# Performance work log

Hardware: AMD Instinct MI355X
Metric: run time of the kernel (lower is better)

Reference implementation:

```python
import jax, jax.numpy as jnp
import numpy as np
import math

L = 6; D = 768; NH = 12; DH = D // NH; V = 2048; CTX = 512; B = 16; T = 512
PAD_ID = 0; PAD_X = 18; PAD_Y = 32; N_ACTIONS = 9


def _layernorm(x, s, b, eps=1e-5):
    m = jnp.mean(x, axis=-1, keepdims=True)
    v = jnp.mean((x - m) ** 2, axis=-1, keepdims=True)
    return (x - m) * jax.lax.rsqrt(v + eps) * s + b


def setup_inputs() -> dict:
    key = jax.random.key(0)
    ks = jax.random.split(key, 16)
    s = 0.02
    x_emb = jax.random.normal(ks[4], (19, D), jnp.float32) * s
    x_emb = x_emb.at[PAD_X].set(0.0)  # padding_idx row is zero in torch
    y_emb = jax.random.normal(ks[5], (33, D), jnp.float32) * s
    y_emb = y_emb.at[PAD_Y].set(0.0)
    return {
        "history_cards": jax.random.randint(ks[0], (B, T), 0, V),
        "history_players": jax.random.randint(ks[1], (B, T), 0, 2),
        "deck": jax.random.randint(ks[2], (B, 8), 0, V),
        "opp_deck": jax.random.randint(ks[3], (B, 8), 0, V),
        "tok_emb": jax.random.normal(ks[6], (V, D), jnp.float32) * s,
        "player_emb": jax.random.normal(ks[7], (2, D), jnp.float32) * s,
        "pos_emb": jax.random.normal(ks[8], (CTX, D), jnp.float32) * s,
        "x_emb": x_emb,
        "y_emb": y_emb,
        "ln1_s": jnp.ones((L, D), jnp.float32),
        "ln1_b": jnp.zeros((L, D), jnp.float32),
        "qkv_w": jax.random.normal(ks[9], (L, D, 3 * D), jnp.float32) * s,
        "qkv_b": jnp.zeros((L, 3 * D), jnp.float32),
        "proj_w": jax.random.normal(ks[10], (L, D, D), jnp.float32) * s,
        "proj_b": jnp.zeros((L, D), jnp.float32),
        "ln2_s": jnp.ones((L, D), jnp.float32),
        "ln2_b": jnp.zeros((L, D), jnp.float32),
        "fc1_w": jax.random.normal(ks[11], (L, D, 4 * D), jnp.float32) * s,
        "fc1_b": jnp.zeros((L, 4 * D), jnp.float32),
        "fc2_w": jax.random.normal(ks[12], (L, 4 * D, D), jnp.float32) * s,
        "fc2_b": jnp.zeros((L, D), jnp.float32),
        "lnf_s": jnp.ones((D,), jnp.float32),
        "lnf_b": jnp.zeros((D,), jnp.float32),
        "head_w": jax.random.normal(ks[13], (D, N_ACTIONS), jnp.float32) * s,
        "head_b": jnp.zeros((N_ACTIONS,), jnp.float32),
    }


def reference(history_cards, history_players, deck, opp_deck,
              tok_emb, player_emb, pos_emb, x_emb, y_emb,
              ln1_s, ln1_b, qkv_w, qkv_b, proj_w, proj_b,
              ln2_s, ln2_b, fc1_w, fc1_b, fc2_w, fc2_b,
              lnf_s, lnf_b, head_w, head_b):
    Bc, Tc = history_cards.shape
    attn_mask = history_cards != PAD_ID                      # (B,T) True = valid
    all_pad = ~jnp.any(attn_mask, axis=1)
    attn_mask = attn_mask.at[:, 0].set(attn_mask[:, 0] | all_pad)

    # multi-embedding sum (history_x/history_y are None => padding rows = 0)
    h = (tok_emb[history_cards]
         + player_emb[jnp.clip(history_players, 0, 1)]
         + x_emb[PAD_X] + y_emb[PAD_Y]
         + jnp.mean(tok_emb[deck], axis=1, keepdims=True)
         + jnp.mean(tok_emb[opp_deck], axis=1, keepdims=True))
    x = h + pos_emb[:Tc][None]                               # (B,T,D)

    causal = jnp.tril(jnp.ones((Tc, Tc), bool))
    mask = causal[None, None, :, :] & attn_mask[:, None, None, :]  # (B,1,T,T)
    neg_inf = jnp.float32(-jnp.inf)
    scale = 1.0 / math.sqrt(DH)

    for i in range(L):
        # attention
        xn = _layernorm(x, ln1_s[i], ln1_b[i])
        qkv = xn @ qkv_w[i] + qkv_b[i]
        q, k, v = jnp.split(qkv, 3, axis=-1)
        q = q.reshape(Bc, Tc, NH, DH)
        k = k.reshape(Bc, Tc, NH, DH)
        v = v.reshape(Bc, Tc, NH, DH)
        scores = jnp.einsum('bihd,bjhd->bhij', q, k) * scale
        scores = jnp.where(mask, scores, neg_inf)
        w = jax.nn.softmax(scores, axis=-1)
        w = jnp.nan_to_num(w, nan=0.0, posinf=0.0, neginf=0.0)
        y = jnp.einsum('bhij,bjhd->bihd', w, v).reshape(Bc, Tc, D)
        x = x + (y @ proj_w[i] + proj_b[i])
        # MLP
        xn = _layernorm(x, ln2_s[i], ln2_b[i])
        hmid = jax.nn.gelu(xn @ fc1_w[i] + fc1_b[i], approximate=False)
        x = x + (hmid @ fc2_w[i] + fc2_b[i])

    x = _layernorm(x, lnf_s, lnf_b)
    last_idx = jnp.clip(jnp.sum(attn_mask.astype(jnp.int32), axis=1) - 1, 0, None)
    last_h = x[jnp.arange(Bc), last_idx]                     # (B,D)
    return last_h @ head_w + head_b                          # (B,9)
```

## Files before the change

### kernel.cpp

```cpp
#include <hip/hip_runtime.h>
#include <hip/hip_bf16.h>
#include <math.h>

typedef __hip_bfloat16 bf16;
typedef __bf16 bf16x8 __attribute__((ext_vector_type(8)));
typedef float f32x4 __attribute__((ext_vector_type(4)));

__device__ __forceinline__ float b2f(bf16 v){ return __bfloat162float(v); }
__device__ __forceinline__ bf16  f2b(float v){ return __float2bfloat16(v); }

__device__ __forceinline__ float gelu_f(float v){
    float y = v * (1.f + 0.044715f * v * v);
    return v / (1.f + __expf(-1.5957691216057308f * y));
}

__device__ __forceinline__ void gl_lds16(const bf16* g, bf16* l) {
    __builtin_amdgcn_global_load_lds((const __attribute__((address_space(1))) unsigned int*)g,
                                     (__attribute__((address_space(3))) unsigned int*)l, 16, 0, 0);
}

__device__ __forceinline__ uint2 pack4bf(const float* v){
    union { unsigned short e[4]; uint2 u; } pk;
    #pragma unroll
    for (int r = 0; r < 4; r++) pk.e[r] = __builtin_bit_cast(unsigned short, f2b(v[r]));
    return pk.u;
}

__device__ __forceinline__ void phase_bar() {
    __builtin_amdgcn_sched_barrier(0);
    __builtin_amdgcn_s_barrier();
    __builtin_amdgcn_sched_barrier(0);
}

__global__ __launch_bounds__(256) void deckmean_k(const int* __restrict__ deck, const int* __restrict__ opp,
                                                  const float* __restrict__ tok, float* __restrict__ deckm)
{
    int b = blockIdx.x, w = blockIdx.y;
    const int* dk = (w ? opp : deck) + b * 8;
    int idx[8];
    #pragma unroll
    for (int j = 0; j < 8; j++) idx[j] = dk[j];
    float* out = deckm + (size_t)(w * 16 + b) * 768;
    for (int d = threadIdx.x; d < 768; d += 256) {
        float s = 0.f;
        #pragma unroll
        for (int j = 0; j < 8; j++) s += tok[(size_t)idx[j] * 768 + d];
        out[d] = s * 0.125f;
    }
}

__global__ __launch_bounds__(512) void mask_k(const int* __restrict__ cards, int* __restrict__ maskb,
                                              int* __restrict__ lastidx)
{
    int b = blockIdx.x, t = threadIdx.x;
    int m = (cards[b * 512 + t] != 0) ? 1 : 0;
    maskb[b * 512 + t] = m;
    __shared__ int red[512];
    red[t] = m; __syncthreads();
    for (int st = 256; st > 0; st >>= 1) { if (t < st) red[t] += red[t + st]; __syncthreads(); }
    if (t == 0) {
        int cnt = red[0];
        if (cnt == 0) { maskb[b * 512] = 1; cnt = 1; }
        lastidx[b] = cnt - 1;
    }
}

__global__ __launch_bounds__(256) void embed_k(const int* __restrict__ cards, const int* __restrict__ players,
                                               const float* __restrict__ tok, const float* __restrict__ pemb,
                                               const float* __restrict__ pos, const float* __restrict__ deckm,
                                               float* __restrict__ x)
{
    int t = blockIdx.x;
    int b = t >> 9, ti = t & 511;
    int cd = cards[t];
    int p = players[t]; p = p < 0 ? 0 : (p > 1 ? 1 : p);
    const float* tr  = tok  + (size_t)cd * 768;
    const float* pr  = pemb + (size_t)p  * 768;
    const float* po  = pos  + (size_t)ti * 768;
    const float* dm = deckm + (size_t)b * 768;
    const float* om = deckm + (size_t)(16 + b) * 768;
    float* xr = x + (size_t)t * 768;
    for (int d = threadIdx.x; d < 768; d += 256)
        xr[d] = tr[d] + pr[d] + po[d] + dm[d] + om[d];
}

__global__ __launch_bounds__(192) void ln_k(const float* __restrict__ x, const float* __restrict__ s,
                                            const float* __restrict__ b, bf16* __restrict__ out)
{
    int row = blockIdx.x, tid = threadIdx.x;
    float4 v = ((const float4*)(x + (size_t)row * 768))[tid];
    float sum = v.x + v.y + v.z + v.w;
    float sq  = v.x * v.x + v.y * v.y + v.z * v.z + v.w * v.w;
    #pragma unroll
    for (int off = 32; off > 0; off >>= 1) {
        sum += __shfl_xor(sum, off, 64);
        sq  += __shfl_xor(sq,  off, 64);
    }
    __shared__ float red[6];
    int wv = tid >> 6;
    if ((tid & 63) == 0) { red[wv] = sum; red[3 + wv] = sq; }
    __syncthreads();
    float S = red[0] + red[1] + red[2];
    float Q = red[3] + red[4] + red[5];
    float mean = S * (1.f / 768.f);
    float var  = Q * (1.f / 768.f) - mean * mean;
    float rstd = rsqrtf(var + 1e-5f);
    float4 sv = ((const float4*)s)[tid];
    float4 bv = ((const float4*)b)[tid];
    float o[4] = { (v.x - mean) * rstd * sv.x + bv.x, (v.y - mean) * rstd * sv.y + bv.y,
                   (v.z - mean) * rstd * sv.z + bv.z, (v.w - mean) * rstd * sv.w + bv.w };
    ((uint2*)(out + (size_t)row * 768))[tid] = pack4bf(o);
}

__global__ __launch_bounds__(256) void transpose4_k(const float* __restrict__ qw, const float* __restrict__ pw,
                                                    const float* __restrict__ f1, const float* __restrict__ f2,
                                                    bf16* __restrict__ oq, bf16* __restrict__ op,
                                                    bf16* __restrict__ o1, bf16* __restrict__ o2)
{
    int t = blockIdx.x;
    const float* in; bf16* out; int K, N, nbx;
    if (t < 432)       { in = qw; out = oq; K = 768;  N = 2304; nbx = 36; }
    else if (t < 576)  { in = pw; out = op; K = 768;  N = 768;  t -= 432;  nbx = 12; }
    else if (t < 1152) { in = f1; out = o1; K = 768;  N = 3072; t -= 576;  nbx = 48; }
    else               { in = f2; out = o2; K = 3072; N = 768;  t -= 1152; nbx = 12; }
    int n0 = (t % nbx) * 64, k0 = (t / nbx) * 64;
    int kq = threadIdx.x & 15, nq = threadIdx.x >> 4;
    float4 rr[4];
    #pragma unroll
    for (int r = 0; r < 4; r++)
        rr[r] = *(const float4*)&in[(size_t)(k0 + kq * 4 + r) * N + n0 + nq * 4];
    const float* fp = (const float*)rr;
    #pragma unroll
    for (int c = 0; c < 4; c++) {
        float v[4] = { fp[c], fp[4 + c], fp[8 + c], fp[12 + c] };
        *(uint2*)&out[(size_t)(n0 + nq * 4 + c) * K + k0 + kq * 4] = pack4bf(v);
    }
}

__global__ __launch_bounds__(512, 2) void gemm256_k(const bf16* __restrict__ A, const bf16* __restrict__ BT,
                                                    const float* __restrict__ bias, bf16* __restrict__ out,
                                                    int N, int K, int act, int nbn)
{
    __shared__ __align__(16) bf16 Asb[2][256 * 64];
    __shared__ __align__(16) bf16 Bsb[2][256 * 64];

    const int tid  = threadIdx.x;
    const int lane = tid & 63, wid = tid >> 6;
    const int quad = lane >> 4, l16 = lane & 15;
    const int wr = wid >> 2, wc = wid & 3;
    const int xr  = l16 & 7;
    const int cg0 = quad ^ xr;
    const int cg1 = cg0 ^ 4;

    const int nwg  = gridDim.x;
    const int wgid = ((int)blockIdx.x & 7) * (nwg >> 3) + ((int)blockIdx.x >> 3);
    const int mt = wgid / nbn, nt = wgid - mt * nbn;
    const int m0 = mt * 256, n0 = nt * 256;

    const int srow = wid * 8 + (lane >> 3);
    const int scg  = (lane & 7) ^ (lane >> 3);
    const bf16* sa[4]; const bf16* sb[4];
    #pragma unroll
    for (int s = 0; s < 4; s++) {
        sa[s] = A  + (size_t)(m0 + s * 64 + srow) * K + scg * 8;
        sb[s] = BT + (size_t)(n0 + s * 64 + srow) * K + scg * 8;
    }

#define STG_A(s, b) gl_lds16(sa[s], &Asb[b][((s) * 64 + wid * 8) * 64])
#define STG_B(s, b) gl_lds16(sb[s], &Bsb[b][((s) * 64 + wid * 8) * 64])
#define LD_B(cg) { _Pragma("unroll") for (int ni = 0; ni < 4; ni++) \
    bfv[ni] = __builtin_bit_cast(bf16x8, *(const uint4*)&Bc[(wc * 64 + ni * 16 + l16) * 64 + (cg) * 8]); }
#define LD_A(rb, cg) { _Pragma("unroll") for (int mi = 0; mi < 4; mi++) \
    afv[mi] = __builtin_bit_cast(bf16x8, *(const uint4*)&Ac[(wr * 128 + (rb) + mi * 16 + l16) * 64 + (cg) * 8]); }
#define MFMA16(MB) { _Pragma("unroll") for (int mi = 0; mi < 4; mi++) \
    _Pragma("unroll") for (int ni = 0; ni < 4; ni++) \
        acc[(MB) + mi][ni] = __builtin_amdgcn_mfma_f32_16x16x32_bf16(bfv[ni], afv[mi], acc[(MB) + mi][ni], 0, 0, 0); }

    STG_A(0, 0); STG_A(2, 0);
    STG_B(0, 0); STG_B(1, 0); STG_B(2, 0); STG_B(3, 0);
    STG_A(1, 0); STG_A(3, 0);
    #pragma unroll
    for (int s = 0; s < 4; s++) { sa[s] += 64; sb[s] += 64; }

    f32x4 acc[8][4] = {};

    asm volatile("s_waitcnt vmcnt(2)" ::: "memory");
    phase_bar();

    const int NKT = K >> 6;
    for (int kt = 0; kt < NKT; kt++) {
        const bf16* Ac = Asb[kt & 1];
        const bf16* Bc = Bsb[kt & 1];
        const int nxt = (kt & 1) ^ 1;
        const bool pf = (kt + 1 < NKT);
        bf16x8 bfv[4], afv[4];

        LD_B(cg0); LD_A(0, cg0);
        if (pf) {
            STG_A(0, nxt); STG_A(2, nxt);
            STG_B(0, nxt); STG_B(1, nxt); STG_B(2, nxt); STG_B(3, nxt);
            asm volatile("s_waitcnt vmcnt(6)" ::: "memory");
        } else {
            asm volatile("s_waitcnt vmcnt(0)" ::: "memory");
        }
        phase_bar();
        __builtin_amdgcn_s_setprio(1); MFMA16(0); __builtin_amdgcn_s_setprio(0);
        phase_bar();

        LD_A(64, cg0);
        if (pf) { STG_A(1, nxt); STG_A(3, nxt); }
        phase_bar();
        __builtin_amdgcn_s_setprio(1); MFMA16(4); __builtin_amdgcn_s_setprio(0);
        phase_bar();

        LD_B(cg1); LD_A(0, cg1);
        phase_bar();
        __builtin_amdgcn_s_setprio(1); MFMA16(0); __builtin_amdgcn_s_setprio(0);
        phase_bar();

        LD_A(64, cg1);
        phase_bar();
        __builtin_amdgcn_s_setprio(1); MFMA16(4); __builtin_amdgcn_s_setprio(0);
        asm volatile("s_waitcnt vmcnt(2)" ::: "memory");
        phase_bar();

        #pragma unroll
        for (int s = 0; s < 4; s++) { sa[s] += 64; sb[s] += 64; }
    }

    float4 bv[4];
    #pragma unroll
    for (int ni = 0; ni < 4; ni++)
        bv[ni] = *(const float4*)&bias[n0 + wc * 64 + ni * 16 + quad * 4];

    #pragma unroll
    for (int mi = 0; mi < 8; mi++) {
        const int m = m0 + wr * 128 + mi * 16 + l16;
        #pragma unroll
        for (int ni = 0; ni < 4; ni++) {
            const int nb2 = n0 + wc * 64 + ni * 16 + quad * 4;
            float v[4] = { acc[mi][ni][0] + bv[ni].x, acc[mi][ni][1] + bv[ni].y,
                           acc[mi][ni][2] + bv[ni].z, acc[mi][ni][3] + bv[ni].w };
            if (act) {
                #pragma unroll
                for (int r = 0; r < 4; r++) v[r] = gelu_f(v[r]);
            }
            *(uint2*)&out[(size_t)m * N + nb2] = pack4bf(v);
        }
    }
#undef STG_A
#undef STG_B
#undef LD_B
#undef LD_A
#undef MFMA16
}

__global__ __launch_bounds__(512, 2) void gemmn128_k(const bf16* __restrict__ A, const bf16* __restrict__ BT,
                                                     const float* __restrict__ bias, float* __restrict__ x,
                                                     int N, int K, int nbn)
{
    __shared__ __align__(16) bf16 Asb[3][256 * 64];
    __shared__ __align__(16) bf16 Bsb[3][128 * 64];

    const int tid  = threadIdx.x;
    const int lane = tid & 63, wid = tid >> 6;
    const int quad = lane >> 4, l16 = lane & 15;
    const int wr = wid >> 1, wc = wid & 1;
    const int cg0 = quad ^ (l16 & 7);
    const int cg1 = cg0 ^ 4;

    const int nwg  = gridDim.x;
    const int wgid = ((int)blockIdx.x & 7) * (nwg >> 3) + ((int)blockIdx.x >> 3);
    const int mt = wgid / nbn, nt = wgid - mt * nbn;
    const int m0 = mt * 256, n0 = nt * 128;

    const int srow = wid * 8 + (lane >> 3);
    const int scg  = (lane & 7) ^ (lane >> 3);
    const bf16* sa[4]; const bf16* sb[2];
    #pragma unroll
    for (int s = 0; s < 4; s++) sa[s] = A  + (size_t)(m0 + s * 64 + srow) * K + scg * 8;
    #pragma unroll
    for (int s = 0; s < 2; s++) sb[s] = BT + (size_t)(n0 + s * 64 + srow) * K + scg * 8;

#define NSTG_A(s, b) gl_lds16(sa[s], &Asb[b][((s) * 64 + wid * 8) * 64])
#define NSTG_B(s, b) gl_lds16(sb[s], &Bsb[b][((s) * 64 + wid * 8) * 64])
#define NSTG6(b) { NSTG_A(0, b); NSTG_A(1, b); NSTG_A(2, b); NSTG_A(3, b); NSTG_B(0, b); NSTG_B(1, b); }
#define NADV { _Pragma("unroll") for (int s = 0; s < 4; s++) sa[s] += 64; sb[0] += 64; sb[1] += 64; }
#define NLD(cg, b) { _Pragma("unroll") for (int i = 0; i < 4; i++) { \
    bfv[i] = __builtin_bit_cast(bf16x8, *(const uint4*)&Bsb[b][(wc * 64 + i * 16 + l16) * 64 + (cg) * 8]); \
    afv[i] = __builtin_bit_cast(bf16x8, *(const uint4*)&Asb[b][(wr * 64 + i * 16 + l16) * 64 + (cg) * 8]); } }
#define NMFMA { _Pragma("unroll") for (int mi = 0; mi < 4; mi++) \
    _Pragma("unroll") for (int ni = 0; ni < 4; ni++) \
        acc[mi][ni] = __builtin_amdgcn_mfma_f32_16x16x32_bf16(bfv[ni], afv[mi], acc[mi][ni], 0, 0, 0); }
#define NITER(CUR, ST) { \
    const bool pf = (kt + 2 < NKT); \
    NLD(cg0, CUR); \
    if (pf) { NSTG6(ST); NADV; } \
    phase_bar(); \
    __builtin_amdgcn_s_setprio(1); NMFMA; __builtin_amdgcn_s_setprio(0); \
    phase_bar(); \
    NLD(cg1, CUR); \
    phase_bar(); \
    __builtin_amdgcn_s_setprio(1); NMFMA; __builtin_amdgcn_s_setprio(0); \
    if (pf)               { asm volatile("s_waitcnt vmcnt(6)" ::: "memory"); phase_bar(); } \
    else if (kt + 1 < NKT){ asm volatile("s_waitcnt vmcnt(0)" ::: "memory"); phase_bar(); } \
    kt++; \
}

    f32x4 acc[4][4] = {};
    const int NKT = K >> 6;

    NSTG6(0); NADV;
    NSTG6(1); NADV;
    asm volatile("s_waitcnt vmcnt(6)" ::: "memory");
    phase_bar();

    int kt = 0;
    bf16x8 bfv[4], afv[4];
    #pragma unroll 1
    for (int kt3 = 0; kt3 < NKT; kt3 += 3) {
        NITER(0, 2);
        NITER(1, 0);
        NITER(2, 1);
    }

    float4 bv4[4];
    #pragma unroll
    for (int ni = 0; ni < 4; ni++)
        bv4[ni] = *(const float4*)&bias[n0 + wc * 64 + ni * 16 + quad * 4];

    #pragma unroll
    for (int mi = 0; mi < 4; mi++) {
        const int m = m0 + wr * 64 + mi * 16 + l16;
        #pragma unroll
        for (int ni = 0; ni < 4; ni++) {
            const int nb2 = n0 + wc * 64 + ni * 16 + quad * 4;
            float* xp = &x[(size_t)m * N + nb2];
            float4 xo = *(float4*)xp;
            xo.x += acc[mi][ni][0] + bv4[ni].x;
            xo.y += acc[mi][ni][1] + bv4[ni].y;
            xo.z += acc[mi][ni][2] + bv4[ni].z;
            xo.w += acc[mi][ni][3] + bv4[ni].w;
            *(float4*)xp = xo;
        }
    }
#undef NSTG_A
#undef NSTG_B
#undef NSTG6
#undef NADV
#undef NLD
#undef NMFMA
#undef NITER
}

__global__ __launch_bounds__(256) void attn_k(const bf16* __restrict__ qkv, const int* __restrict__ mask,
                                              bf16* __restrict__ y)
{
    const int qt = blockIdx.x, h = blockIdx.y, b = blockIdx.z;
    const int qbase = qt * 128, tokb = b * 512;
    __shared__ __align__(16) unsigned short Kl[128][72];
    __shared__ __align__(16) unsigned short Vt[64][136];
    __shared__ __align__(16) unsigned short Ptq[4][16][136];
    __shared__ float mkf[128];

    const int tid = threadIdx.x, wave = tid >> 6, lane = tid & 63;
    const int quad = lane >> 4, l16 = lane & 15;

    bf16x8 bq[2][2];
    #pragma unroll
    for (int qc = 0; qc < 2; qc++) {
        const bf16* qp = &qkv[(size_t)(tokb + qbase + wave * 32 + qc * 16 + l16) * 2304 + h * 64];
        bq[qc][0] = __builtin_bit_cast(bf16x8, *(const uint4*)(qp + quad * 8));
        bq[qc][1] = __builtin_bit_cast(bf16x8, *(const uint4*)(qp + 32 + quad * 8));
    }

    float m_i[2] = { -INFINITY, -INFINITY }, l_i[2] = { 0.f, 0.f };
    f32x4 Oacc[2][4] = {};

    const int nst = qt + 1;
    for (int s = 0; s < nst; s++) {
        const int j0 = s * 128;
        __syncthreads();
        {
            int key = tid >> 1, c0 = (tid & 1) * 32;
            const bf16* kg = &qkv[(size_t)(tokb + j0 + key) * 2304 + 768  + h * 64 + c0];
            const bf16* vg = &qkv[(size_t)(tokb + j0 + key) * 2304 + 1536 + h * 64 + c0];
            #pragma unroll
            for (int q = 0; q < 4; q++)
                *(uint4*)&Kl[key][c0 + q * 8] = *(const uint4*)(kg + q * 8);
            union { uint4 u[4]; unsigned short e[32]; } vv;
            #pragma unroll
            for (int q = 0; q < 4; q++) vv.u[q] = *(const uint4*)(vg + q * 8);
            #pragma unroll
            for (int j = 0; j < 32; j++) Vt[c0 + j][key] = vv.e[j];
            if (tid < 128) mkf[tid] = mask[b * 512 + j0 + tid] ? 0.f : -INFINITY;
        }
        __syncthreads();

        #pragma unroll
        for (int qc = 0; qc < 2; qc++) {
            const int qi = qbase + wave * 32 + qc * 16 + l16;

            f32x4 sc[8] = {};
            #pragma unroll
            for (int kcc = 0; kcc < 8; kcc++) {
                bf16x8 af0 = __builtin_bit_cast(bf16x8, *(const uint4*)&Kl[kcc * 16 + l16][quad * 8]);
                bf16x8 af1 = __builtin_bit_cast(bf16x8, *(const uint4*)&Kl[kcc * 16 + l16][32 + quad * 8]);
                sc[kcc] = __builtin_amdgcn_mfma_f32_16x16x32_bf16(af0, bq[qc][0], sc[kcc], 0, 0, 0);
                sc[kcc] = __builtin_amdgcn_mfma_f32_16x16x32_bf16(af1, bq[qc][1], sc[kcc], 0, 0, 0);
            }

            float pv[8][4];
            float mx = -INFINITY;
            #pragma unroll
            for (int kcc = 0; kcc < 8; kcc++) {
                float4 mk4 = *(const float4*)&mkf[kcc * 16 + quad * 4];
                float mkr[4] = { mk4.x, mk4.y, mk4.z, mk4.w };
                #pragma unroll
                for (int r = 0; r < 4; r++) {
                    int krel = kcc * 16 + quad * 4 + r;
                    float sval = (j0 + krel <= qi) ? (sc[kcc][r] * 0.125f + mkr[r]) : -INFINITY;
                    pv[kcc][r] = sval;
                    mx = fmaxf(mx, sval);
                }
            }
            mx = fmaxf(mx, __shfl_xor(mx, 16, 64));
            mx = fmaxf(mx, __shfl_xor(mx, 32, 64));
            float mn = fmaxf(m_i[qc], mx);
            float alpha = (mn == -INFINITY) ? 1.f : __expf(m_i[qc] - mn);
            float lsum = 0.f;
            #pragma unroll
            for (int kcc = 0; kcc < 8; kcc++)
                #pragma unroll
                for (int r = 0; r < 4; r++) {
                    float pp = (pv[kcc][r] == -INFINITY) ? 0.f : __expf(pv[kcc][r] - mn);
                    pv[kcc][r] = pp; lsum += pp;
                }
            lsum += __shfl_xor(lsum, 16, 64);
            lsum += __shfl_xor(lsum, 32, 64);
            m_i[qc] = mn; l_i[qc] = alpha * l_i[qc] + lsum;

            #pragma unroll
            for (int kcc = 0; kcc < 8; kcc++)
                *(uint2*)&Ptq[wave][l16][kcc * 16 + quad * 4] = pack4bf(pv[kcc]);
            #pragma unroll
            for (int mc = 0; mc < 4; mc++)
                #pragma unroll
                for (int r = 0; r < 4; r++) Oacc[qc][mc][r] *= alpha;

            __syncthreads();

            #pragma unroll
            for (int kcc = 0; kcc < 4; kcc++) {
                bf16x8 pb = __builtin_bit_cast(bf16x8, *(const uint4*)&Ptq[wave][l16][kcc * 32 + quad * 8]);
                #pragma unroll
                for (int mc = 0; mc < 4; mc++) {
                    bf16x8 vf = __builtin_bit_cast(bf16x8, *(const uint4*)&Vt[mc * 16 + l16][kcc * 32 + quad * 8]);
                    Oacc[qc][mc] = __builtin_amdgcn_mfma_f32_16x16x32_bf16(vf, pb, Oacc[qc][mc], 0, 0, 0);
                }
            }
        }
    }

    #pragma unroll
    for (int qc = 0; qc < 2; qc++) {
        float inv = (l_i[qc] > 0.f) ? 1.f / l_i[qc] : 0.f;
        const int tok = tokb + qbase + wave * 32 + qc * 16 + l16;
        #pragma unroll
        for (int mc = 0; mc < 4; mc++) {
            float v[4] = { Oacc[qc][mc][0] * inv, Oacc[qc][mc][1] * inv,
                           Oacc[qc][mc][2] * inv, Oacc[qc][mc][3] * inv };
            *(uint2*)&y[(size_t)tok * 768 + h * 64 + mc * 16 + quad * 4] = pack4bf(v);
        }
    }
}

__global__ __launch_bounds__(256) void head_k(const float* __restrict__ x, const int* __restrict__ lastidx,
                                              const float* __restrict__ ls, const float* __restrict__ lb,
                                              const float* __restrict__ hw, const float* __restrict__ hb,
                                              float* __restrict__ out)
{
    int b = blockIdx.x, tid = threadIdx.x;
    const float* xr = x + ((size_t)(b * 512 + lastidx[b])) * 768;
    float v0 = xr[tid], v1 = xr[tid + 256], v2 = xr[tid + 512];
    __shared__ float rs[256], rq[256];
    rs[tid] = v0 + v1 + v2; rq[tid] = v0 * v0 + v1 * v1 + v2 * v2;
    __syncthreads();
    for (int st = 128; st > 0; st >>= 1) {
        if (tid < st) { rs[tid] += rs[tid + st]; rq[tid] += rq[tid + st]; }
        __syncthreads();
    }
    float mean = rs[0] * (1.f / 768.f);
    float var  = rq[0] * (1.f / 768.f) - mean * mean;
    float rstd = rsqrtf(var + 1e-5f);
    float part[9];
    #pragma unroll
    for (int a = 0; a < 9; a++) part[a] = 0.f;
    float vv[3] = { v0, v1, v2 };
    #pragma unroll
    for (int e = 0; e < 3; e++) {
        int d = tid + e * 256;
        float xnv = (vv[e] - mean) * rstd * ls[d] + lb[d];
        #pragma unroll
        for (int a = 0; a < 9; a++) part[a] += xnv * hw[d * 9 + a];
    }
    __shared__ float r9[9][256];
    #pragma unroll
    for (int a = 0; a < 9; a++) r9[a][tid] = part[a];
    __syncthreads();
    for (int st = 128; st > 0; st >>= 1) {
        if (tid < st) {
            for (int a = 0; a < 9; a++) r9[a][tid] += r9[a][tid + st];
        }
        __syncthreads();
    }
    if (tid < 9) out[b * 9 + tid] = r9[tid][0] + hb[tid];
}

extern "C" void kernel_launch(void* const* d_in, const int* in_sizes, int n_in,
                              void* d_out, int out_size, void* d_ws, size_t ws_size,
                              hipStream_t stream) {
    const int*   cards   = (const int*)  d_in[0];
    const int*   players = (const int*)  d_in[1];
    const int*   deck    = (const int*)  d_in[2];
    const int*   oppd    = (const int*)  d_in[3];
    const float* tok     = (const float*)d_in[4];
    const float* pemb    = (const float*)d_in[5];
    const float* pos     = (const float*)d_in[6];
    const float* ln1s  = (const float*)d_in[9];
    const float* ln1b  = (const float*)d_in[10];
    const float* qkvw  = (const float*)d_in[11];
    const float* qkvb  = (const float*)d_in[12];
    const float* projw = (const float*)d_in[13];
    const float* projb = (const float*)d_in[14];
    const float* ln2s  = (const float*)d_in[15];
    const float* ln2b  = (const float*)d_in[16];
    const float* fc1w  = (const float*)d_in[17];
    const float* fc1b  = (const float*)d_in[18];
    const float* fc2w  = (const float*)d_in[19];
    const float* fc2b  = (const float*)d_in[20];
    const float* lnfs  = (const float*)d_in[21];
    const float* lnfb  = (const float*)d_in[22];
    const float* hw    = (const float*)d_in[23];
    const float* hb    = (const float*)d_in[24];
    float* out = (float*)d_out;

    char* p = (char*)d_ws;
    auto alloc = [&](size_t bytes) { char* q = p; p += (bytes + 255) & ~((size_t)255); return q; };
    float* x     = (float*)alloc(8192ull * 768 * 4);
    bf16*  xn    = (bf16*) alloc(8192ull * 768 * 2);
    bf16*  big   = (bf16*) alloc(8192ull * 3072 * 2);
    bf16*  wt    = (bf16*) alloc(7077888ull * 2);
    float* deckm = (float*)alloc(2ull * 16 * 768 * 4);
    int*   maskb = (int*)  alloc(8192ull * 4);
    int*   lasti = (int*)  alloc(64);

    bf16* wq = wt;
    bf16* wp = wq + 2304ull * 768;
    bf16* w1 = wp + 768ull * 768;
    bf16* w2 = w1 + 3072ull * 768;

    deckmean_k<<<dim3(16, 2), 256, 0, stream>>>(deck, oppd, tok, deckm);
    mask_k<<<16, 512, 0, stream>>>(cards, maskb, lasti);
    embed_k<<<8192, 256, 0, stream>>>(cards, players, tok, pemb, pos, deckm, x);

    for (int i = 0; i < 6; i++) {
        transpose4_k<<<1728, 256, 0, stream>>>(
            qkvw + (size_t)i * 768 * 2304, projw + (size_t)i * 768 * 768,
            fc1w + (size_t)i * 768 * 3072, fc2w + (size_t)i * 3072 * 768,
            wq, wp, w1, w2);

        ln_k<<<8192, 192, 0, stream>>>(x, ln1s + i * 768, ln1b + i * 768, xn);
        gemm256_k<<<288, 512, 0, stream>>>(xn, wq, qkvb + i * 2304, big, 2304, 768, 0, 9);
        attn_k<<<dim3(4, 12, 16), 256, 0, stream>>>(big, maskb, xn);
        gemmn128_k<<<192, 512, 0, stream>>>(xn, wp, projb + i * 768, x, 768, 768, 6);
        ln_k<<<8192, 192, 0, stream>>>(x, ln2s + i * 768, ln2b + i * 768, xn);
        gemm256_k<<<384, 512, 0, stream>>>(xn, w1, fc1b + i * 3072, big, 3072, 768, 1, 12);
        gemmn128_k<<<192, 512, 0, stream>>>(big, w2, fc2b + i * 768, x, 768, 3072, 6);
    }

    head_k<<<16, 256, 0, stream>>>(x, lasti, lnfs, lnfb, hw, hb, out);
}
```

Measured before the change: 1.971 ms.

## Reorder GEMM k-loop to reuse B fragments and prefetch A two tiles ahead

```diff
diff --git a/kernel.cpp b/kernel.cpp
--- a/kernel.cpp
+++ b/kernel.cpp
@@ -168,64 +168,63 @@
 
 #define STG_A(s, b) gl_lds16(sa[s], &Asb[b][((s) * 64 + wid * 8) * 64])
 #define STG_B(s, b) gl_lds16(sb[s], &Bsb[b][((s) * 64 + wid * 8) * 64])
-#define LD_B(cg) { _Pragma("unroll") for (int ni = 0; ni < 4; ni++) \
-    bfv[ni] = __builtin_bit_cast(bf16x8, *(const uint4*)&Bc[(wc * 64 + ni * 16 + l16) * 64 + (cg) * 8]); }
+#define ADV { _Pragma("unroll") for (int s = 0; s < 4; s++) { sa[s] += 64; sb[s] += 64; } }
+#define LD_B(BV, cg) { _Pragma("unroll") for (int ni = 0; ni < 4; ni++) \
+    BV[ni] = __builtin_bit_cast(bf16x8, *(const uint4*)&Bc[(wc * 64 + ni * 16 + l16) * 64 + (cg) * 8]); }
 #define LD_A(rb, cg) { _Pragma("unroll") for (int mi = 0; mi < 4; mi++) \
     afv[mi] = __builtin_bit_cast(bf16x8, *(const uint4*)&Ac[(wr * 128 + (rb) + mi * 16 + l16) * 64 + (cg) * 8]); }
-#define MFMA16(MB) { _Pragma("unroll") for (int mi = 0; mi < 4; mi++) \
+#define MFMA16(MB, BV) { _Pragma("unroll") for (int mi = 0; mi < 4; mi++) \
     _Pragma("unroll") for (int ni = 0; ni < 4; ni++) \
-        acc[(MB) + mi][ni] = __builtin_amdgcn_mfma_f32_16x16x32_bf16(bfv[ni], afv[mi], acc[(MB) + mi][ni], 0, 0, 0); }
-
-    STG_A(0, 0); STG_A(2, 0);
+        acc[(MB) + mi][ni] = __builtin_amdgcn_mfma_f32_16x16x32_bf16(BV[ni], afv[mi], acc[(MB) + mi][ni], 0, 0, 0); }
+
+    f32x4 acc[8][4] = {};
+    const int NKT = K >> 6;
+
+    STG_A(0, 0); STG_A(2, 0); STG_A(1, 0); STG_A(3, 0);
     STG_B(0, 0); STG_B(1, 0); STG_B(2, 0); STG_B(3, 0);
-    STG_A(1, 0); STG_A(3, 0);
-    #pragma unroll
-    for (int s = 0; s < 4; s++) { sa[s] += 64; sb[s] += 64; }
-
-    f32x4 acc[8][4] = {};
-
-    asm volatile("s_waitcnt vmcnt(2)" ::: "memory");
+    ADV;
+    if (NKT > 1) {
+        STG_A(0, 1); STG_A(2, 1);
+        asm volatile("s_waitcnt vmcnt(2)" ::: "memory");
+    } else {
+        asm volatile("s_waitcnt vmcnt(0)" ::: "memory");
+    }
     phase_bar();
 
-    const int NKT = K >> 6;
     for (int kt = 0; kt < NKT; kt++) {
         const bf16* Ac = Asb[kt & 1];
         const bf16* Bc = Bsb[kt & 1];
-        const int nxt = (kt & 1) ^ 1;
-        const bool pf = (kt + 1 < NKT);
-        bf16x8 bfv[4], afv[4];
-
-        LD_B(cg0); LD_A(0, cg0);
-        if (pf) {
-            STG_A(0, nxt); STG_A(2, nxt);
-            STG_B(0, nxt); STG_B(1, nxt); STG_B(2, nxt); STG_B(3, nxt);
-            asm volatile("s_waitcnt vmcnt(6)" ::: "memory");
-        } else {
-            asm volatile("s_waitcnt vmcnt(0)" ::: "memory");
-        }
-        phase_bar();
-        __builtin_amdgcn_s_setprio(1); MFMA16(0); __builtin_amdgcn_s_setprio(0);
+        const int cur = kt & 1, oth = cur ^ 1;
+        const bool pf1 = (kt + 1 < NKT), pf2 = (kt + 2 < NKT);
+        bf16x8 bfv0[4], bfv1[4], afv[4];
+
+        LD_B(bfv0, cg0); LD_A(0, cg0);
+        if (pf1) {
+            STG_B(0, oth); STG_B(1, oth); STG_B(2, oth); STG_B(3, oth);
+            STG_A(1, oth); STG_A(3, oth);
+        }
+        ADV;
+        phase_bar();
+        __builtin_amdgcn_s_setprio(1); MFMA16(0, bfv0); __builtin_amdgcn_s_setprio(0);
+        phase_bar();
+
+        LD_B(bfv1, cg1); LD_A(0, cg1);
+        phase_bar();
+        __builtin_amdgcn_s_setprio(1); MFMA16(0, bfv1); __builtin_amdgcn_s_setprio(0);
         phase_bar();
 
         LD_A(64, cg0);
-        if (pf) { STG_A(1, nxt); STG_A(3, nxt); }
-        phase_bar();
-        __builtin_amdgcn_s_setprio(1); MFMA16(4); __builtin_amdgcn_s_setprio(0);
-        phase_bar();
-
-        LD_B(cg1); LD_A(0, cg1);
-        phase_bar();
-        __builtin_amdgcn_s_setprio(1); MFMA16(0); __builtin_amdgcn_s_setprio(0);
+        if (pf2) { STG_A(0, cur); STG_A(2, cur); }
+        phase_bar();
+        __builtin_amdgcn_s_setprio(1); MFMA16(4, bfv0); __builtin_amdgcn_s_setprio(0);
         phase_bar();
 
         LD_A(64, cg1);
         phase_bar();
-        __builtin_amdgcn_s_setprio(1); MFMA16(4); __builtin_amdgcn_s_setprio(0);
-        asm volatile("s_waitcnt vmcnt(2)" ::: "memory");
-        phase_bar();
-
-        #pragma unroll
-        for (int s = 0; s < 4; s++) { sa[s] += 64; sb[s] += 64; }
+        __builtin_amdgcn_s_setprio(1); MFMA16(4, bfv1); __builtin_amdgcn_s_setprio(0);
+        if (pf2)      { asm volatile("s_waitcnt vmcnt(2)" ::: "memory"); }
+        else if (pf1) { asm volatile("s_waitcnt vmcnt(0)" ::: "memory"); }
+        phase_bar();
     }
 
     float4 bv[4];
@@ -250,6 +249,7 @@
     }
 #undef STG_A
 #undef STG_B
+#undef ADV
 #undef LD_B
 #undef LD_A
 #undef MFMA16
```

After: 1.996 ms. No clear change (+1.3%).
